# Performance work log

Measured on AMD Instinct MI355X. Metric: run time of the kernel, lower is better.

The kernel has to match this reference:

```python
import jax, jax.numpy as jnp
import numpy as np

C_IN, H, W = 8, 32, 32
C_OUT, K, S, P = 32, 4, 2, 1
HO = (H + 2 * P - K) // S + 1  # 16
WO = (W + 2 * P - K) // S + 1  # 16
IN_FEAT = C_IN * H * W          # 8192
OUT_FEAT = C_OUT * HO * WO      # 8192


def conv2d(x, w, b=None):
    # x: [N, C_in, H, W], w: [C_out, C_in, K, K]
    y = jax.lax.conv_general_dilated(
        x, w, window_strides=(S, S), padding=[(P, P), (P, P)],
        dimension_numbers=("NCHW", "OIHW", "NCHW"))
    if b is not None:
        y = y + b[None, :, None, None]
    return y


def toeplitz_matrix(weight):
    # Equivalent to torch.autograd.functional.jacobian of flatten(conv(x)):
    # conv is linear, so apply it to the identity basis (batched conv).
    eye = jnp.eye(IN_FEAT, dtype=weight.dtype).reshape(IN_FEAT, C_IN, H, W)
    cols = conv2d(eye, weight).reshape(IN_FEAT, OUT_FEAT)  # column j = conv(e_j)
    return cols.T  # [OUT_FEAT, IN_FEAT]


def setup_inputs() -> dict:
    key = jax.random.key(0)
    k1, k2, k3, k4 = jax.random.split(key, 4)
    center = jax.random.normal(k1, (C_IN, H, W), jnp.float32)
    eps = 0.01 * jax.random.uniform(k2, (C_IN, H, W), jnp.float32)
    bounds = jnp.stack([center - eps, center + eps], 0)  # [2, C_in, H, W]
    weight = 0.1 * jax.random.normal(k3, (C_OUT, C_IN, K, K), jnp.float32)
    bias = 0.1 * jax.random.normal(k4, (C_OUT,), jnp.float32)
    assignment = jnp.zeros((C_OUT, HO, WO), jnp.int32)  # unused by forward
    return {"bounds": bounds, "weight": weight, "bias": bias,
            "assignment": assignment}


def reference(bounds, weight, bias, assignment):
    W_plus = jnp.maximum(weight, 0.0)
    W_minus = jnp.minimum(weight, 0.0)
    half_b = bias / 2.0
    l = bounds[0][None]  # [1, C_in, H, W]
    u = bounds[1][None]
    # upper = conv_plus(u) + conv_minus(l); each conv carries bias/2
    upper = conv2d(u, W_plus, half_b) + conv2d(l, W_minus, half_b)
    lower = conv2d(l, W_plus, half_b) + conv2d(u, W_minus, half_b)
    out_bounds = jnp.concatenate([lower, upper], 0)  # [2, C_out, HO, WO]

    # back-substitution (terminal branch: predecessor is the input layer)
    W_mat = toeplitz_matrix(weight)                 # [OUT_FEAT, IN_FEAT]
    bias_backsub = jnp.repeat(bias, HO * WO)        # repeat_interleave
    Mp = jnp.maximum(W_mat, 0.0)
    Mm = jnp.minimum(W_mat, 0.0)
    lf = bounds[0].reshape(-1)
    uf = bounds[1].reshape(-1)
    new_l = (Mp @ lf + Mm @ uf + bias_backsub).reshape(C_OUT, HO, WO)
    new_u = (Mp @ uf + Mm @ lf + bias_backsub).reshape(C_OUT, HO, WO)
    # tighten: keep the better of forward-propagated and back-substituted
    out_bounds = out_bounds.at[0].set(jnp.where(new_l > out_bounds[0], new_l, out_bounds[0]))
    out_bounds = out_bounds.at[1].set(jnp.where(new_u < out_bounds[1], new_u, out_bounds[1]))
    return out_bounds, W_mat, bias_backsub
```

## Files before the change

kernel.cpp:

```cpp
#include <hip/hip_runtime.h>

#define C_IN   8
#define HH     32
#define WW     32
#define C_OUT  32
#define KK     4
#define SS     2
#define PP     1
#define HO     16
#define WO     16
#define IN_FEAT  8192
#define OUT_FEAT 8192

typedef float v4f __attribute__((ext_vector_type(4)));

__global__ __launch_bounds__(256) void wmat_kernel(const float* __restrict__ weight,
                                                   float* __restrict__ wmat) {
    const int idx = blockIdx.x * 256 + threadIdx.x;
    const int row = idx >> 11;
    const int col = (idx & 2047) << 2;

    const int c_out = row >> 8;
    const int ho    = (row >> 4) & 15;
    const int wo    = row & 15;

    const int c_in  = col >> 10;
    const int h     = (col >> 5) & 31;
    const int w0    = col & 31;

    const int kh  = h  - (ho * 2 - 1);
    const int kwb = w0 - (wo * 2 - 1);

    float v[4] = {0.f, 0.f, 0.f, 0.f};
    if ((unsigned)kh < (unsigned)KK) {
        const float* wrow = weight + ((c_out * C_IN + c_in) * (KK * KK) + kh * KK);
#pragma unroll
        for (int j = 0; j < 4; ++j) {
            const int kw = kwb + j;
            if ((unsigned)kw < (unsigned)KK) v[j] = wrow[kw];
        }
    }
    v4f o = { v[0], v[1], v[2], v[3] };
    __builtin_nontemporal_store(o, reinterpret_cast<v4f*>(wmat) + idx);
}

__global__ __launch_bounds__(256) void bounds_kernel(const float* __restrict__ bounds,
                                                     const float* __restrict__ weight,
                                                     const float* __restrict__ bias,
                                                     float* __restrict__ out_bounds,
                                                     float* __restrict__ bias_bs) {
    const int t = blockIdx.x * 256 + threadIdx.x;
    const int c_out = t >> 8;
    const int ho    = (t >> 4) & 15;
    const int wo    = t & 15;

    const float* lptr = bounds;
    const float* uptr = bounds + C_IN * HH * WW;

    float lo = 0.f, up = 0.f;
    for (int ci = 0; ci < C_IN; ++ci) {
#pragma unroll
        for (int kh = 0; kh < KK; ++kh) {
            const int h = ho * SS - PP + kh;
            if ((unsigned)h >= (unsigned)HH) continue;
#pragma unroll
            for (int kw = 0; kw < KK; ++kw) {
                const int w = wo * SS - PP + kw;
                if ((unsigned)w >= (unsigned)WW) continue;
                const float wv = weight[(c_out * C_IN + ci) * (KK * KK) + kh * KK + kw];
                const float wp = fmaxf(wv, 0.f);
                const float wm = fminf(wv, 0.f);
                const int off = ci * (HH * WW) + h * WW + w;
                const float lv = lptr[off];
                const float uv = uptr[off];
                lo = fmaf(wp, lv, lo); lo = fmaf(wm, uv, lo);
                up = fmaf(wp, uv, up); up = fmaf(wm, lv, up);
            }
        }
    }
    const float b = bias[c_out];
    out_bounds[t]            = lo + b;
    out_bounds[OUT_FEAT + t] = up + b;
    bias_bs[t] = b;
}

extern "C" void kernel_launch(void* const* d_in, const int* in_sizes, int n_in,
                              void* d_out, int out_size, void* d_ws, size_t ws_size,
                              hipStream_t stream) {
    const float* bounds = (const float*)d_in[0];
    const float* weight = (const float*)d_in[1];
    const float* bias   = (const float*)d_in[2];

    float* out     = (float*)d_out;
    float* wmat    = out + 2 * OUT_FEAT;
    float* bias_bs = out + 2 * OUT_FEAT + (size_t)OUT_FEAT * IN_FEAT;

    wmat_kernel<<<65536, 256, 0, stream>>>(weight, wmat);
    bounds_kernel<<<32, 256, 0, stream>>>(bounds, weight, bias, out, bias_bs);
}
```

Before: 287.4 us.

## Zero-fill Toeplitz matrix, then scatter nonzero weights with fused wave-reduced bounds

The dense per-element construction of the 8192x8192 Toeplitz matrix is replaced by a plain float4 zero-fill kernel. A second kernel follows, where each 64-lane wave handles one output row: it scatters the row's at most 128 nonzero weights into the matrix and computes the interval bounds with a shuffle reduction. This removes per-element index arithmetic and weight lookups from the large write, and spreads the bounds work across far more threads. In exchange it adds a second pass of uncoalesced scattered stores after the fill, and it drops the nontemporal store hint.

```diff
diff --git a/kernel.cpp b/kernel.cpp
--- a/kernel.cpp
+++ b/kernel.cpp
@@ -12,76 +12,62 @@
 #define IN_FEAT  8192
 #define OUT_FEAT 8192
 
-typedef float v4f __attribute__((ext_vector_type(4)));
+__global__ __launch_bounds__(256) void zero_wmat(float4* __restrict__ wmat) {
+    const int stride = 16384 * 256;
+    int idx = blockIdx.x * 256 + threadIdx.x;
+#pragma unroll
+    for (int it = 0; it < 4; ++it, idx += stride)
+        wmat[idx] = make_float4(0.f, 0.f, 0.f, 0.f);
+}
 
-__global__ __launch_bounds__(256) void wmat_kernel(const float* __restrict__ weight,
-                                                   float* __restrict__ wmat) {
-    const int idx = blockIdx.x * 256 + threadIdx.x;
-    const int row = idx >> 11;
-    const int col = (idx & 2047) << 2;
+__global__ __launch_bounds__(256) void scatter_bounds(const float* __restrict__ bounds,
+                                                      const float* __restrict__ weight,
+                                                      const float* __restrict__ bias,
+                                                      float* __restrict__ wmat,
+                                                      float* __restrict__ out_bounds,
+                                                      float* __restrict__ bias_bs) {
+    const int row  = (blockIdx.x * 256 + threadIdx.x) >> 6;
+    const int lane = threadIdx.x & 63;
 
     const int c_out = row >> 8;
     const int ho    = (row >> 4) & 15;
     const int wo    = row & 15;
 
-    const int c_in  = col >> 10;
-    const int h     = (col >> 5) & 31;
-    const int w0    = col & 31;
+    const float* lptr = bounds;
+    const float* uptr = bounds + IN_FEAT;
 
-    const int kh  = h  - (ho * 2 - 1);
-    const int kwb = w0 - (wo * 2 - 1);
-
-    float v[4] = {0.f, 0.f, 0.f, 0.f};
-    if ((unsigned)kh < (unsigned)KK) {
-        const float* wrow = weight + ((c_out * C_IN + c_in) * (KK * KK) + kh * KK);
+    float lo = 0.f, up = 0.f;
 #pragma unroll
-        for (int j = 0; j < 4; ++j) {
-            const int kw = kwb + j;
-            if ((unsigned)kw < (unsigned)KK) v[j] = wrow[kw];
+    for (int s = 0; s < 2; ++s) {
+        const int t  = lane + 64 * s;
+        const int ci = t >> 4;
+        const int kh = (t >> 2) & 3;
+        const int kw = t & 3;
+        const int h  = ho * SS - PP + kh;
+        const int w  = wo * SS - PP + kw;
+        if ((unsigned)h < (unsigned)HH && (unsigned)w < (unsigned)WW) {
+            const float wv  = weight[(c_out * C_IN + ci) * (KK * KK) + kh * KK + kw];
+            const int   col = ci * (HH * WW) + h * WW + w;
+            wmat[(size_t)row * IN_FEAT + col] = wv;
+            const float lv = lptr[col];
+            const float uv = uptr[col];
+            const float wp = fmaxf(wv, 0.f);
+            const float wm = fminf(wv, 0.f);
+            lo = fmaf(wp, lv, fmaf(wm, uv, lo));
+            up = fmaf(wp, uv, fmaf(wm, lv, up));
         }
     }
-    v4f o = { v[0], v[1], v[2], v[3] };
-    __builtin_nontemporal_store(o, reinterpret_cast<v4f*>(wmat) + idx);
-}
-
-__global__ __launch_bounds__(256) void bounds_kernel(const float* __restrict__ bounds,
-                                                     const float* __restrict__ weight,
-                                                     const float* __restrict__ bias,
-                                                     float* __restrict__ out_bounds,
-                                                     float* __restrict__ bias_bs) {
-    const int t = blockIdx.x * 256 + threadIdx.x;
-    const int c_out = t >> 8;
-    const int ho    = (t >> 4) & 15;
-    const int wo    = t & 15;
-
-    const float* lptr = bounds;
-    const float* uptr = bounds + C_IN * HH * WW;
-
-    float lo = 0.f, up = 0.f;
-    for (int ci = 0; ci < C_IN; ++ci) {
 #pragma unroll
-        for (int kh = 0; kh < KK; ++kh) {
-            const int h = ho * SS - PP + kh;
-            if ((unsigned)h >= (unsigned)HH) continue;
-#pragma unroll
-            for (int kw = 0; kw < KK; ++kw) {
-                const int w = wo * SS - PP + kw;
-                if ((unsigned)w >= (unsigned)WW) continue;
-                const float wv = weight[(c_out * C_IN + ci) * (KK * KK) + kh * KK + kw];
-                const float wp = fmaxf(wv, 0.f);
-                const float wm = fminf(wv, 0.f);
-                const int off = ci * (HH * WW) + h * WW + w;
-                const float lv = lptr[off];
-                const float uv = uptr[off];
-                lo = fmaf(wp, lv, lo); lo = fmaf(wm, uv, lo);
-                up = fmaf(wp, uv, up); up = fmaf(wm, lv, up);
-            }
-        }
+    for (int off = 32; off; off >>= 1) {
+        lo += __shfl_down(lo, off, 64);
+        up += __shfl_down(up, off, 64);
     }
-    const float b = bias[c_out];
-    out_bounds[t]            = lo + b;
-    out_bounds[OUT_FEAT + t] = up + b;
-    bias_bs[t] = b;
+    if (lane == 0) {
+        const float b = bias[c_out];
+        out_bounds[row]            = lo + b;
+        out_bounds[OUT_FEAT + row] = up + b;
+        bias_bs[row] = b;
+    }
 }
 
 extern "C" void kernel_launch(void* const* d_in, const int* in_sizes, int n_in,
@@ -95,6 +81,6 @@
     float* wmat    = out + 2 * OUT_FEAT;
     float* bias_bs = out + 2 * OUT_FEAT + (size_t)OUT_FEAT * IN_FEAT;
 
-    wmat_kernel<<<65536, 256, 0, stream>>>(weight, wmat);
-    bounds_kernel<<<32, 256, 0, stream>>>(bounds, weight, bias, out, bias_bs);
+    zero_wmat<<<16384, 256, 0, stream>>>((float4*)wmat);
+    scatter_bounds<<<2048, 256, 0, stream>>>(bounds, weight, bias, wmat, out, bias_bs);
 }
```

Result: faster. 264.9 us (-7.8%).
